# Performance work log

Hardware: AMD Instinct MI355X
Metric: run time of the kernel (lower is better)

Reference implementation:

```python
import jax, jax.numpy as jnp
import numpy as np


def setup_inputs() -> dict:
    key = jax.random.key(0)
    ks = jax.random.split(key, 7)
    B, P, D = 32, 576, 768   # batch, tokens (24x24 patches), inp_dim
    H, HD = 12, 64           # n_heads, head_dim = inp_dim // n_heads
    s = 0.02
    return {
        "x": jax.random.normal(ks[0], (B, P, D), dtype=jnp.float32),
        "Wq": jax.random.normal(ks[1], (H, D, HD), dtype=jnp.float32) * s,
        "bq": jax.random.normal(ks[2], (H, HD), dtype=jnp.float32) * s,
        "Wk": jax.random.normal(ks[3], (H, D, HD), dtype=jnp.float32) * s,
        "bk": jax.random.normal(ks[4], (H, HD), dtype=jnp.float32) * s,
        "Wv": jax.random.normal(ks[5], (H, D, HD), dtype=jnp.float32) * s,
        "bv": jax.random.normal(ks[6], (H, HD), dtype=jnp.float32) * s,
    }


def reference(x, Wq, bq, Wk, bk, Wv, bv):
    # Per-head independent linear projections (stacked over head axis h).
    # x: [b, p, d]; Wq/Wk/Wv: [h, d, k]; biases: [h, k]
    q = jnp.einsum("bpd,hdk->bhpk", x, Wq) + bq[None, :, None, :]
    k = jnp.einsum("bpd,hdk->bhpk", x, Wk) + bk[None, :, None, :]
    v = jnp.einsum("bpd,hdk->bhpk", x, Wv) + bv[None, :, None, :]
    head_dim = k.shape[-1]
    scale = 1.0 / jnp.sqrt(jnp.asarray(head_dim, dtype=x.dtype))
    attn = jnp.einsum("bhqk,bhpk->bhqp", q, k) * scale  # [b, h, p, p]
    attn = jax.nn.softmax(attn, axis=-1)
    out = jnp.einsum("bhqp,bhpk->bhqk", attn, v)        # [b, h, p, k]
    b, h, p, hd = out.shape
    # concat heads along last dim (dropout is identity in eval mode)
    return jnp.transpose(out, (0, 2, 1, 3)).reshape(b, p, h * hd)
```

## Files before the change

### kernel.cpp

```cpp
#include <hip/hip_runtime.h>

typedef unsigned short ushort_t;
typedef unsigned int u32;
typedef float f32x4 __attribute__((ext_vector_type(4)));
typedef short short8 __attribute__((ext_vector_type(8)));

#define NB 32
#define NP 576
#define ND 768
#define NH 12
#define NHD 64

#define WT_BYTES  (36*64*768*2)
#define KV_BYTES  (32*12*576*64*2)
#define QSCALE    0.18033688f

static __device__ __forceinline__ ushort_t f2bf(float f) {
    return __builtin_bit_cast(ushort_t, (__bf16)f);
}
static __device__ __forceinline__ short8 pack8(float4 a, float4 b) {
    union { ushort_t u[8]; short8 v; } pk;
    pk.u[0]=f2bf(a.x); pk.u[1]=f2bf(a.y); pk.u[2]=f2bf(a.z); pk.u[3]=f2bf(a.w);
    pk.u[4]=f2bf(b.x); pk.u[5]=f2bf(b.y); pk.u[6]=f2bf(b.z); pk.u[7]=f2bf(b.w);
    return pk.v;
}
static __device__ __forceinline__ void gl_lds16(const ushort_t* g, ushort_t* l) {
    __builtin_amdgcn_global_load_lds((const __attribute__((address_space(1))) u32*)g,
                                     (__attribute__((address_space(3))) u32*)l, 16, 0, 0);
}
static __device__ __forceinline__ int swzb(int row, int chunk) {
    return row * 128 + (((chunk ^ (row & 7)) & 7) << 4);
}
#define MFMA16 __builtin_amdgcn_mfma_f32_16x16x32_bf16

__global__ __launch_bounds__(256) void prep_w(
    const float* __restrict__ Wq, const float* __restrict__ Wk,
    const float* __restrict__ Wv, ushort_t* __restrict__ Wt)
{
    int idx = blockIdx.x * 256 + threadIdx.x;
    int d0   = (idx % 96) * 8;
    int rest = idx / 96;
    int hd   = rest & 63;
    int ph   = rest >> 6;
    int h    = ph % 12, pr = ph / 12;
    const float* W = (pr == 0) ? Wq : (pr == 1 ? Wk : Wv);
    union { ushort_t u[8]; short8 v; } pk;
    #pragma unroll
    for (int j = 0; j < 8; ++j)
        pk.u[j] = f2bf(W[(size_t)(h * 768 + d0 + j) * 64 + hd]);
    *(short8*)(Wt + ((size_t)(ph * 64 + hd)) * 768 + d0) = pk.v;
}

__global__ __launch_bounds__(256) void proj_qkv(
    const float* __restrict__ x, const ushort_t* __restrict__ Wt,
    const float* __restrict__ bq, const float* __restrict__ bk,
    const float* __restrict__ bv,
    ushort_t* __restrict__ Qb, ushort_t* __restrict__ Kb,
    ushort_t* __restrict__ Vtb, int nts, int ph_base)
{
    __shared__ ushort_t smem[22528];

    const int t = threadIdx.x;
    const int w = t >> 6, l = t & 63, m16 = l & 15, g = l >> 4;
    const int wm = w >> 1, wn = w & 1;

    int L = blockIdx.y * gridDim.x + blockIdx.x;
    int xcd = L & 7, jj_ = L >> 3;
    int nt = jj_ % nts, mt = (jj_ / nts) * 8 + xcd;
    const int m0 = mt * 96;
    const int b  = mt / 6, pb = (mt % 6) * 96;

    const int grow = l >> 3, gch = (l & 7) ^ grow;

    float4 ar[3][2];
    auto loadA = [&](int kc) {
        #pragma unroll
        for (int q = 0; q < 3; ++q) {
            int c = t + q * 256, row = c >> 3, ch = c & 7;
            const float4* xp = (const float4*)(x + (size_t)(m0 + row) * 768 + kc * 64 + ch * 8);
            ar[q][0] = xp[0]; ar[q][1] = xp[1];
        }
    };
    auto writeA = [&]() {
        #pragma unroll
        for (int q = 0; q < 3; ++q) {
            int c = t + q * 256, row = c >> 3, ch = c & 7;
            *(short8*)((char*)smem + swzb(row, ch)) = pack8(ar[q][0], ar[q][1]);
        }
    };
    auto stageB = [&](int kc, int d) {
        #pragma unroll
        for (int c4 = 0; c4 < 4; ++c4) {
            int ci = w * 4 + c4;
            const ushort_t* gs = Wt + (size_t)(ph_base * 64 + nt * 128 + ci * 8 + grow) * 768
                               + kc * 64 + gch * 8;
            gl_lds16(gs, smem + 6144 + d * 8192 + ci * 512);
        }
    };

    f32x4 acc[3][4] = {};

    loadA(0); stageB(0, 0); writeA();
    __syncthreads();

    for (int kc = 0; kc < 12; ++kc) {
        const int d = kc & 1;
        if (kc < 11) { loadA(kc + 1); stageB(kc + 1, d ^ 1); }
        __builtin_amdgcn_s_setprio(1);
        #pragma unroll
        for (int jj = 0; jj < 2; ++jj) {
            short8 af[3], bf[4];
            #pragma unroll
            for (int mi = 0; mi < 3; ++mi)
                af[mi] = *(const short8*)((char*)smem + swzb(wm * 48 + mi * 16 + m16, jj * 4 + g));
            #pragma unroll
            for (int ni = 0; ni < 4; ++ni)
                bf[ni] = *(const short8*)((char*)smem + 12288 + d * 16384 + swzb(wn * 64 + ni * 16 + m16, jj * 4 + g));
            #pragma unroll
            for (int mi = 0; mi < 3; ++mi)
                #pragma unroll
                for (int ni = 0; ni < 4; ++ni)
                    acc[mi][ni] = MFMA16(af[mi], bf[ni], acc[mi][ni], 0, 0, 0);
        }
        __builtin_amdgcn_s_setprio(0);
        __syncthreads();
        if (kc < 11) {
            writeA();
            __syncthreads();
        }
    }

    const int ph = ph_base + nt * 2 + wn;
    const int proj = ph / 12, h = ph % 12;
    const float* bias = (proj == 0 ? bq : (proj == 1 ? bk : bv)) + h * 64;
    const float qs = (proj == 0) ? QSCALE : 1.0f;
    ushort_t* sE = smem + w * 4608;

    #pragma unroll
    for (int ni = 0; ni < 4; ++ni) {
        float bvv = bias[ni * 16 + m16];
        #pragma unroll
        for (int mi = 0; mi < 3; ++mi)
            #pragma unroll
            for (int i = 0; i < 4; ++i) {
                float val = (acc[mi][ni][i] + bvv) * qs;
                int tok = mi * 16 + g * 4 + i;
                int hd  = ni * 16 + m16;
                if (proj < 2) sE[tok * 72 + hd] = f2bf(val);
                else          sE[hd * 72 + tok] = f2bf(val);
            }
    }
    if (proj < 2) {
        ushort_t* dst = (proj == 0 ? Qb : Kb)
                      + ((size_t)(b * 12 + h) * 576 + pb + wm * 48) * 64;
        #pragma unroll
        for (int rr = 0; rr < 6; ++rr) {
            int row = rr * 8 + (l >> 3), ch = l & 7;
            *(short8*)(dst + (size_t)row * 64 + ch * 8) = *(const short8*)&sE[row * 72 + ch * 8];
        }
    } else {
        ushort_t* dst = Vtb + (size_t)(b * 12 + h) * 64 * 576 + pb + wm * 48;
        #pragma unroll
        for (int rr = 0; rr < 8; ++rr) {
            int hd = rr * 8 + (l >> 3), tc = l & 7;
            if (tc < 6)
                *(short8*)(dst + (size_t)hd * 576 + tc * 8) = *(const short8*)&sE[hd * 72 + tc * 8];
        }
    }
}

template<int FUSEQ>
__global__ __launch_bounds__(256) void attn_k(
    const float* __restrict__ x, const ushort_t* __restrict__ Wt,
    const float* __restrict__ bq, const ushort_t* __restrict__ Qb,
    const ushort_t* __restrict__ Kb, const ushort_t* __restrict__ Vtb,
    float* __restrict__ out)
{
    __shared__ ushort_t smem[20480];

    const int t = threadIdx.x;
    const int w = t >> 6, l = t & 63, m16 = l & 15, g = l >> 4;

    int L = blockIdx.y * 9 + blockIdx.x;
    int xcd = L & 7, jj_ = L >> 3;
    int qt = jj_ % 9, bh = (jj_ / 9) * 8 + xcd;
    const int b = bh / 12, h = bh % 12;
    const int p0 = qt * 64;

    const int grow = l >> 3, gch = (l & 7) ^ grow;
    const int spbase = 32768 + w * 2048;

    short8 aq0, aq1;

    if constexpr (FUSEQ) {
        f32x4 acc[4] = {};
        const int row = t >> 2, c16 = (t & 3) * 16;
        auto stage = [&](int kc, int d) {
            const float4* xp = (const float4*)(x + (size_t)(b * 576 + p0 + row) * 768 + kc * 64 + c16);
            float4 u0 = xp[0], u1 = xp[1], u2 = xp[2], u3 = xp[3];
            *(short8*)((char*)smem + d * 8192 + swzb(row, c16 >> 3))       = pack8(u0, u1);
            *(short8*)((char*)smem + d * 8192 + swzb(row, (c16 >> 3) + 1)) = pack8(u2, u3);
            #pragma unroll
            for (int c2 = 0; c2 < 2; ++c2) {
                int ci = w * 2 + c2;
                const ushort_t* gs = Wt + (size_t)(h * 64 + ci * 8 + grow) * 768 + kc * 64 + gch * 8;
                gl_lds16(gs, smem + (16384 + d * 8192 + ci * 1024) / 2);
            }
        };
        stage(0, 0); __syncthreads();
        for (int kc = 0; kc < 12; ++kc) {
            int d = kc & 1;
            if (kc < 11) stage(kc + 1, d ^ 1);
            __builtin_amdgcn_s_setprio(1);
            #pragma unroll
            for (int jj = 0; jj < 2; ++jj) {
                short8 a = *(const short8*)((char*)smem + d * 8192 + swzb(w * 16 + m16, jj * 4 + g));
                #pragma unroll
                for (int f = 0; f < 4; ++f) {
                    short8 bb = *(const short8*)((char*)smem + 16384 + d * 8192 + swzb(f * 16 + m16, jj * 4 + g));
                    acc[f] = MFMA16(a, bb, acc[f], 0, 0, 0);
                }
            }
            __builtin_amdgcn_s_setprio(0);
            __syncthreads();
        }
        #pragma unroll
        for (int f = 0; f < 4; ++f) {
            float bqv = bq[h * 64 + f * 16 + m16];
            #pragma unroll
            for (int i = 0; i < 4; ++i) {
                float val = (acc[f][i] + bqv) * QSCALE;
                int r = g * 4 + i, c = f * 16 + m16;
                *(ushort_t*)((char*)smem + spbase + r * 128
                    + (((((c >> 3) ^ (r & 7)) & 7) << 4) | ((c & 7) << 1))) = f2bf(val);
            }
        }
        aq0 = *(const short8*)((char*)smem + spbase + m16 * 128 + (((g ^ (m16 & 7)) & 7) << 4));
        aq1 = *(const short8*)((char*)smem + spbase + m16 * 128 + ((((4 + g) ^ (m16 & 7)) & 7) << 4));
    } else {
        const ushort_t* qsrc = Qb + ((size_t)bh * 576 + p0 + w * 16 + m16) * 64 + g * 8;
        aq0 = *(const short8*)qsrc;
        aq1 = *(const short8*)(qsrc + 32);
    }

    const ushort_t* Kbase = Kb  + (size_t)bh * (576 * 64);
    const ushort_t* Vbase = Vtb + (size_t)bh * (64 * 576);

    auto stageKV = [&](int kt, int d) {
        #pragma unroll
        for (int c2 = 0; c2 < 2; ++c2) {
            int ci = w * 2 + c2;
            gl_lds16(Kbase + (size_t)(kt * 64 + ci * 8 + grow) * 64 + gch * 8,
                     smem + (d * 8192 + ci * 1024) / 2);
            gl_lds16(Vbase + (size_t)(ci * 8 + grow) * 576 + kt * 64 + gch * 8,
                     smem + (16384 + d * 8192 + ci * 1024) / 2);
        }
    };

    float psum[4] = {0.f, 0.f, 0.f, 0.f};
    f32x4 accO[4] = {};

    stageKV(0, 0); __syncthreads();
    for (int kt = 0; kt < 9; ++kt) {
        int d = kt & 1;
        if (kt < 8) stageKV(kt + 1, d ^ 1);

        f32x4 s[4] = {};
        __builtin_amdgcn_s_setprio(1);
        #pragma unroll
        for (int jj = 0; jj < 2; ++jj) {
            short8 aqj = jj ? aq1 : aq0;
            #pragma unroll
            for (int f = 0; f < 4; ++f) {
                short8 bk_ = *(const short8*)((char*)smem + d * 8192 + swzb(f * 16 + m16, jj * 4 + g));
                s[f] = MFMA16(aqj, bk_, s[f], 0, 0, 0);
            }
        }
        __builtin_amdgcn_s_setprio(0);

        #pragma unroll
        for (int f = 0; f < 4; ++f)
            #pragma unroll
            for (int i = 0; i < 4; ++i) {
                float p = exp2f(s[f][i]);
                s[f][i] = p;
                psum[i] += p;
            }

        #pragma unroll
        for (int f = 0; f < 4; ++f)
            #pragma unroll
            for (int i = 0; i < 4; ++i) {
                int r = g * 4 + i, c = f * 16 + m16;
                *(ushort_t*)((char*)smem + spbase + r * 128
                    + (((((c >> 3) ^ (r & 7)) & 7) << 4) | ((c & 7) << 1))) = f2bf(s[f][i]);
            }
        short8 pa0 = *(const short8*)((char*)smem + spbase + m16 * 128 + (((g ^ (m16 & 7)) & 7) << 4));
        short8 pa1 = *(const short8*)((char*)smem + spbase + m16 * 128 + ((((4 + g) ^ (m16 & 7)) & 7) << 4));

        __builtin_amdgcn_s_setprio(1);
        #pragma unroll
        for (int jj = 0; jj < 2; ++jj) {
            short8 paj = jj ? pa1 : pa0;
            #pragma unroll
            for (int f = 0; f < 4; ++f) {
                short8 bv_ = *(const short8*)((char*)smem + 16384 + d * 8192 + swzb(f * 16 + m16, jj * 4 + g));
                accO[f] = MFMA16(paj, bv_, accO[f], 0, 0, 0);
            }
        }
        __builtin_amdgcn_s_setprio(0);
        __syncthreads();
    }

    #pragma unroll
    for (int xm = 1; xm < 16; xm <<= 1)
        #pragma unroll
        for (int i = 0; i < 4; ++i)
            psum[i] += __shfl_xor(psum[i], xm, 64);

    float inv[4];
    #pragma unroll
    for (int i = 0; i < 4; ++i) inv[i] = 1.0f / psum[i];
    float* orow = out + ((size_t)b * 576 + p0 + w * 16) * 768 + h * 64;
    #pragma unroll
    for (int f = 0; f < 4; ++f)
        #pragma unroll
        for (int i = 0; i < 4; ++i)
            orow[(size_t)(g * 4 + i) * 768 + f * 16 + m16] = accO[f][i] * inv[i];
}

extern "C" void kernel_launch(void* const* d_in, const int* in_sizes, int n_in,
                              void* d_out, int out_size, void* d_ws, size_t ws_size,
                              hipStream_t stream) {
    const float* x  = (const float*)d_in[0];
    const float* Wq = (const float*)d_in[1];
    const float* bq = (const float*)d_in[2];
    const float* Wk = (const float*)d_in[3];
    const float* bk = (const float*)d_in[4];
    const float* Wv = (const float*)d_in[5];
    const float* bv = (const float*)d_in[6];
    float* out = (float*)d_out;

    ushort_t* Wt  = (ushort_t*)d_ws;
    ushort_t* Kb  = (ushort_t*)((char*)d_ws + WT_BYTES);
    ushort_t* Vtb = (ushort_t*)((char*)d_ws + WT_BYTES + KV_BYTES);
    ushort_t* Qb  = (ushort_t*)((char*)d_ws + WT_BYTES + 2 * (size_t)KV_BYTES);

    const bool bigws = ws_size >= (size_t)WT_BYTES + 3 * (size_t)KV_BYTES;

    hipLaunchKernelGGL(prep_w, dim3(864), dim3(256), 0, stream, Wq, Wk, Wv, Wt);
    if (bigws) {
        hipLaunchKernelGGL(proj_qkv, dim3(18, 192), dim3(256), 0, stream,
                           x, Wt, bq, bk, bv, Qb, Kb, Vtb, 18, 0);
        hipLaunchKernelGGL((attn_k<0>), dim3(9, 384), dim3(256), 0, stream,
                           x, Wt, bq, Qb, Kb, Vtb, out);
    } else {
        hipLaunchKernelGGL(proj_qkv, dim3(12, 192), dim3(256), 0, stream,
                           x, Wt, bq, bk, bv, Qb, Kb, Vtb, 12, 12);
        hipLaunchKernelGGL((attn_k<1>), dim3(9, 384), dim3(256), 0, stream,
                           x, Wt, bq, Qb, Kb, Vtb, out);
    }
}
```

Before: 196.5 us.

## Pre-convert x to bf16, fuse Q projection into attention, use async-staged KV projection

Adds a prep pass that converts x to bf16 alongside the weight transpose. The K/V projection becomes a 128x128-tile kernel that loads both operands with global_load_lds. The Q projection is dropped from the projection kernel and computed inside the attention kernel from the bf16 x via async loads. This removes the Q round-trip through memory and the fp32 x reloads with in-register conversion, at the cost of an extra bf16 copy of x and a non-double-buffered projection loop.

```diff
diff --git a/kernel.cpp b/kernel.cpp
--- a/kernel.cpp
+++ b/kernel.cpp
@@ -5,13 +5,8 @@
 typedef float f32x4 __attribute__((ext_vector_type(4)));
 typedef short short8 __attribute__((ext_vector_type(8)));
 
-#define NB 32
-#define NP 576
-#define ND 768
-#define NH 12
-#define NHD 64
-
 #define WT_BYTES  (36*64*768*2)
+#define XB_BYTES  (32*576*768*2)
 #define KV_BYTES  (32*12*576*64*2)
 #define QSCALE    0.18033688f
 
@@ -33,40 +28,145 @@
 }
 #define MFMA16 __builtin_amdgcn_mfma_f32_16x16x32_bf16
 
-__global__ __launch_bounds__(256) void prep_w(
+__global__ __launch_bounds__(256) void prep(
     const float* __restrict__ Wq, const float* __restrict__ Wk,
-    const float* __restrict__ Wv, ushort_t* __restrict__ Wt)
+    const float* __restrict__ Wv, const float* __restrict__ x,
+    ushort_t* __restrict__ Wt, ushort_t* __restrict__ xb)
 {
     int idx = blockIdx.x * 256 + threadIdx.x;
-    int d0   = (idx % 96) * 8;
-    int rest = idx / 96;
-    int hd   = rest & 63;
-    int ph   = rest >> 6;
-    int h    = ph % 12, pr = ph / 12;
-    const float* W = (pr == 0) ? Wq : (pr == 1 ? Wk : Wv);
-    union { ushort_t u[8]; short8 v; } pk;
-    #pragma unroll
-    for (int j = 0; j < 8; ++j)
-        pk.u[j] = f2bf(W[(size_t)(h * 768 + d0 + j) * 64 + hd]);
-    *(short8*)(Wt + ((size_t)(ph * 64 + hd)) * 768 + d0) = pk.v;
-}
-
-__global__ __launch_bounds__(256) void proj_qkv(
-    const float* __restrict__ x, const ushort_t* __restrict__ Wt,
-    const float* __restrict__ bq, const float* __restrict__ bk,
-    const float* __restrict__ bv,
-    ushort_t* __restrict__ Qb, ushort_t* __restrict__ Kb,
-    ushort_t* __restrict__ Vtb, int nts, int ph_base)
+    if (idx < 221184) {
+        int d0   = (idx % 96) * 8;
+        int rest = idx / 96;
+        int hd   = rest & 63;
+        int ph   = rest >> 6;
+        int h    = ph % 12, pr = ph / 12;
+        const float* W = (pr == 0) ? Wq : (pr == 1 ? Wk : Wv);
+        union { ushort_t u[8]; short8 v; } pk;
+        #pragma unroll
+        for (int j = 0; j < 8; ++j)
+            pk.u[j] = f2bf(W[(size_t)(h * 768 + d0 + j) * 64 + hd]);
+        *(short8*)(Wt + ((size_t)(ph * 64 + hd)) * 768 + d0) = pk.v;
+    } else {
+        size_t e = (size_t)(idx - 221184) * 8;
+        const float4* xp = (const float4*)(x + e);
+        *(short8*)(xb + e) = pack8(xp[0], xp[1]);
+    }
+}
+
+__global__ __launch_bounds__(256) void proj_kv(
+    const ushort_t* __restrict__ xb, const ushort_t* __restrict__ Wt,
+    const float* __restrict__ bk, const float* __restrict__ bv,
+    ushort_t* __restrict__ Kb, ushort_t* __restrict__ Vtb)
 {
-    __shared__ ushort_t smem[22528];
+    __shared__ ushort_t smem[18432];
 
     const int t = threadIdx.x;
     const int w = t >> 6, l = t & 63, m16 = l & 15, g = l >> 4;
     const int wm = w >> 1, wn = w & 1;
 
-    int L = blockIdx.y * gridDim.x + blockIdx.x;
+    int L = blockIdx.y * 12 + blockIdx.x;
     int xcd = L & 7, jj_ = L >> 3;
-    int nt = jj_ % nts, mt = (jj_ / nts) * 8 + xcd;
+    int nt = jj_ % 12, mt = (jj_ / 12) * 8 + xcd;
+    const int m0 = mt * 128;
+    const int ph0 = 12 + nt * 2;
+
+    const int grow = l >> 3, gch = (l & 7) ^ grow;
+
+    auto stageA = [&](int kc) {
+        #pragma unroll
+        for (int c4 = 0; c4 < 4; ++c4) {
+            int ci = w * 4 + c4;
+            gl_lds16(xb + (size_t)(m0 + ci * 8 + grow) * 768 + kc * 64 + gch * 8,
+                     smem + ci * 512);
+        }
+    };
+    auto stageB = [&](int kc) {
+        #pragma unroll
+        for (int c4 = 0; c4 < 4; ++c4) {
+            int ci = w * 4 + c4;
+            int r  = ci * 8 + grow;
+            gl_lds16(Wt + ((size_t)(ph0 + (r >> 6)) * 64 + (r & 63)) * 768 + kc * 64 + gch * 8,
+                     smem + 8192 + ci * 512);
+        }
+    };
+
+    f32x4 acc[4][4] = {};
+
+    for (int kc = 0; kc < 12; ++kc) {
+        __syncthreads();
+        stageA(kc); stageB(kc);
+        __syncthreads();
+        __builtin_amdgcn_s_setprio(1);
+        #pragma unroll
+        for (int jj = 0; jj < 2; ++jj) {
+            short8 af[4], bf[4];
+            #pragma unroll
+            for (int mi = 0; mi < 4; ++mi)
+                af[mi] = *(const short8*)((char*)smem + swzb(wm * 64 + mi * 16 + m16, jj * 4 + g));
+            #pragma unroll
+            for (int ni = 0; ni < 4; ++ni)
+                bf[ni] = *(const short8*)((char*)smem + 16384 + swzb(wn * 64 + ni * 16 + m16, jj * 4 + g));
+            #pragma unroll
+            for (int mi = 0; mi < 4; ++mi)
+                #pragma unroll
+                for (int ni = 0; ni < 4; ++ni)
+                    acc[mi][ni] = MFMA16(af[mi], bf[ni], acc[mi][ni], 0, 0, 0);
+        }
+        __builtin_amdgcn_s_setprio(0);
+    }
+    __syncthreads();
+
+    const int ph = ph0 + wn, proj = ph / 12, h = ph % 12;
+    const float* bias = (proj == 1 ? bk : bv) + h * 64;
+    const int tokg0 = m0 + wm * 64;
+    const int bb = tokg0 / 576, pp = tokg0 % 576;
+    ushort_t* sE = smem + w * 4608;
+
+    #pragma unroll
+    for (int ni = 0; ni < 4; ++ni) {
+        float bvv = bias[ni * 16 + m16];
+        #pragma unroll
+        for (int mi = 0; mi < 4; ++mi)
+            #pragma unroll
+            for (int i = 0; i < 4; ++i) {
+                float val = acc[mi][ni][i] + bvv;
+                int tok = mi * 16 + g * 4 + i;
+                int hd  = ni * 16 + m16;
+                if (proj == 1) sE[tok * 72 + hd] = f2bf(val);
+                else           sE[hd * 72 + tok] = f2bf(val);
+            }
+    }
+    if (proj == 1) {
+        ushort_t* dst = Kb + ((size_t)(bb * 12 + h) * 576 + pp) * 64;
+        #pragma unroll
+        for (int rr = 0; rr < 8; ++rr) {
+            int row = rr * 8 + (l >> 3), ch = l & 7;
+            *(short8*)(dst + (size_t)row * 64 + ch * 8) = *(const short8*)&sE[row * 72 + ch * 8];
+        }
+    } else {
+        ushort_t* dst = Vtb + (size_t)(bb * 12 + h) * 64 * 576 + pp;
+        #pragma unroll
+        for (int rr = 0; rr < 8; ++rr) {
+            int hd = rr * 8 + (l >> 3), tc = l & 7;
+            *(short8*)(dst + (size_t)hd * 576 + tc * 8) = *(const short8*)&sE[hd * 72 + tc * 8];
+        }
+    }
+}
+
+__global__ __launch_bounds__(256) void proj_reg(
+    const float* __restrict__ x, const ushort_t* __restrict__ Wt,
+    const float* __restrict__ bk, const float* __restrict__ bv,
+    ushort_t* __restrict__ Kb, ushort_t* __restrict__ Vtb)
+{
+    __shared__ ushort_t smem[22528];
+
+    const int t = threadIdx.x;
+    const int w = t >> 6, l = t & 63, m16 = l & 15, g = l >> 4;
+    const int wm = w >> 1, wn = w & 1;
+
+    int L = blockIdx.y * 12 + blockIdx.x;
+    int xcd = L & 7, jj_ = L >> 3;
+    int nt = jj_ % 12, mt = (jj_ / 12) * 8 + xcd;
     const int m0 = mt * 96;
     const int b  = mt / 6, pb = (mt % 6) * 96;
 
@@ -92,14 +192,13 @@
         #pragma unroll
         for (int c4 = 0; c4 < 4; ++c4) {
             int ci = w * 4 + c4;
-            const ushort_t* gs = Wt + (size_t)(ph_base * 64 + nt * 128 + ci * 8 + grow) * 768
+            const ushort_t* gs = Wt + (size_t)((12 + nt * 2) * 64 + ci * 8 + grow) * 768
                                + kc * 64 + gch * 8;
             gl_lds16(gs, smem + 6144 + d * 8192 + ci * 512);
         }
     };
 
     f32x4 acc[3][4] = {};
-
     loadA(0); stageB(0, 0); writeA();
     __syncthreads();
 
@@ -124,16 +223,12 @@
         }
         __builtin_amdgcn_s_setprio(0);
         __syncthreads();
-        if (kc < 11) {
-            writeA();
-            __syncthreads();
-        }
-    }
-
-    const int ph = ph_base + nt * 2 + wn;
+        if (kc < 11) { writeA(); __syncthreads(); }
+    }
+
+    const int ph = 12 + nt * 2 + wn;
     const int proj = ph / 12, h = ph % 12;
-    const float* bias = (proj == 0 ? bq : (proj == 1 ? bk : bv)) + h * 64;
-    const float qs = (proj == 0) ? QSCALE : 1.0f;
+    const float* bias = (proj == 1 ? bk : bv) + h * 64;
     ushort_t* sE = smem + w * 4608;
 
     #pragma unroll
@@ -143,16 +238,15 @@
         for (int mi = 0; mi < 3; ++mi)
             #pragma unroll
             for (int i = 0; i < 4; ++i) {
-                float val = (acc[mi][ni][i] + bvv) * qs;
+                float val = acc[mi][ni][i] + bvv;
                 int tok = mi * 16 + g * 4 + i;
                 int hd  = ni * 16 + m16;
-                if (proj < 2) sE[tok * 72 + hd] = f2bf(val);
-                else          sE[hd * 72 + tok] = f2bf(val);
-            }
-    }
-    if (proj < 2) {
-        ushort_t* dst = (proj == 0 ? Qb : Kb)
-                      + ((size_t)(b * 12 + h) * 576 + pb + wm * 48) * 64;
+                if (proj == 1) sE[tok * 72 + hd] = f2bf(val);
+                else           sE[hd * 72 + tok] = f2bf(val);
+            }
+    }
+    if (proj == 1) {
+        ushort_t* dst = Kb + ((size_t)(b * 12 + h) * 576 + pb + wm * 48) * 64;
         #pragma unroll
         for (int rr = 0; rr < 6; ++rr) {
             int row = rr * 8 + (l >> 3), ch = l & 7;
@@ -169,10 +263,10 @@
     }
 }
 
-template<int FUSEQ>
+template<int MODE>
 __global__ __launch_bounds__(256) void attn_k(
-    const float* __restrict__ x, const ushort_t* __restrict__ Wt,
-    const float* __restrict__ bq, const ushort_t* __restrict__ Qb,
+    const float* __restrict__ x, const ushort_t* __restrict__ xb,
+    const ushort_t* __restrict__ Wt, const float* __restrict__ bq,
     const ushort_t* __restrict__ Kb, const ushort_t* __restrict__ Vtb,
     float* __restrict__ out)
 {
@@ -191,20 +285,30 @@
     const int spbase = 32768 + w * 2048;
 
     short8 aq0, aq1;
-
-    if constexpr (FUSEQ) {
+    {
         f32x4 acc[4] = {};
-        const int row = t >> 2, c16 = (t & 3) * 16;
         auto stage = [&](int kc, int d) {
-            const float4* xp = (const float4*)(x + (size_t)(b * 576 + p0 + row) * 768 + kc * 64 + c16);
-            float4 u0 = xp[0], u1 = xp[1], u2 = xp[2], u3 = xp[3];
-            *(short8*)((char*)smem + d * 8192 + swzb(row, c16 >> 3))       = pack8(u0, u1);
-            *(short8*)((char*)smem + d * 8192 + swzb(row, (c16 >> 3) + 1)) = pack8(u2, u3);
-            #pragma unroll
-            for (int c2 = 0; c2 < 2; ++c2) {
-                int ci = w * 2 + c2;
-                const ushort_t* gs = Wt + (size_t)(h * 64 + ci * 8 + grow) * 768 + kc * 64 + gch * 8;
-                gl_lds16(gs, smem + (16384 + d * 8192 + ci * 1024) / 2);
+            if constexpr (MODE == 2) {
+                #pragma unroll
+                for (int c2 = 0; c2 < 2; ++c2) {
+                    int ci = w * 2 + c2;
+                    gl_lds16(xb + (size_t)(b * 576 + p0 + ci * 8 + grow) * 768 + kc * 64 + gch * 8,
+                             smem + (d * 8192 + ci * 1024) / 2);
+                    gl_lds16(Wt + (size_t)(h * 64 + ci * 8 + grow) * 768 + kc * 64 + gch * 8,
+                             smem + (16384 + d * 8192 + ci * 1024) / 2);
+                }
+            } else {
+                const int row = t >> 2, c16 = (t & 3) * 16;
+                const float4* xp = (const float4*)(x + (size_t)(b * 576 + p0 + row) * 768 + kc * 64 + c16);
+                float4 u0 = xp[0], u1 = xp[1], u2 = xp[2], u3 = xp[3];
+                *(short8*)((char*)smem + d * 8192 + swzb(row, c16 >> 3))       = pack8(u0, u1);
+                *(short8*)((char*)smem + d * 8192 + swzb(row, (c16 >> 3) + 1)) = pack8(u2, u3);
+                #pragma unroll
+                for (int c2 = 0; c2 < 2; ++c2) {
+                    int ci = w * 2 + c2;
+                    gl_lds16(Wt + (size_t)(h * 64 + ci * 8 + grow) * 768 + kc * 64 + gch * 8,
+                             smem + (16384 + d * 8192 + ci * 1024) / 2);
+                }
             }
         };
         stage(0, 0); __syncthreads();
@@ -237,10 +341,6 @@
         }
         aq0 = *(const short8*)((char*)smem + spbase + m16 * 128 + (((g ^ (m16 & 7)) & 7) << 4));
         aq1 = *(const short8*)((char*)smem + spbase + m16 * 128 + ((((4 + g) ^ (m16 & 7)) & 7) << 4));
-    } else {
-        const ushort_t* qsrc = Qb + ((size_t)bh * 576 + p0 + w * 16 + m16) * 64 + g * 8;
-        aq0 = *(const short8*)qsrc;
-        aq1 = *(const short8*)(qsrc + 32);
     }
 
     const ushort_t* Kbase = Kb  + (size_t)bh * (576 * 64);
@@ -341,23 +441,26 @@
     const float* bv = (const float*)d_in[6];
     float* out = (float*)d_out;
 
-    ushort_t* Wt  = (ushort_t*)d_ws;
-    ushort_t* Kb  = (ushort_t*)((char*)d_ws + WT_BYTES);
-    ushort_t* Vtb = (ushort_t*)((char*)d_ws + WT_BYTES + KV_BYTES);
-    ushort_t* Qb  = (ushort_t*)((char*)d_ws + WT_BYTES + 2 * (size_t)KV_BYTES);
-
-    const bool bigws = ws_size >= (size_t)WT_BYTES + 3 * (size_t)KV_BYTES;
-
-    hipLaunchKernelGGL(prep_w, dim3(864), dim3(256), 0, stream, Wq, Wk, Wv, Wt);
+    const bool bigws = ws_size >= (size_t)WT_BYTES + XB_BYTES + 2 * (size_t)KV_BYTES;
+
     if (bigws) {
-        hipLaunchKernelGGL(proj_qkv, dim3(18, 192), dim3(256), 0, stream,
-                           x, Wt, bq, bk, bv, Qb, Kb, Vtb, 18, 0);
-        hipLaunchKernelGGL((attn_k<0>), dim3(9, 384), dim3(256), 0, stream,
-                           x, Wt, bq, Qb, Kb, Vtb, out);
+        ushort_t* Wt  = (ushort_t*)d_ws;
+        ushort_t* xbp = (ushort_t*)((char*)d_ws + WT_BYTES);
+        ushort_t* Kb  = (ushort_t*)((char*)d_ws + WT_BYTES + XB_BYTES);
+        ushort_t* Vtb = (ushort_t*)((char*)d_ws + WT_BYTES + XB_BYTES + (size_t)KV_BYTES);
+        hipLaunchKernelGGL(prep, dim3(7776), dim3(256), 0, stream, Wq, Wk, Wv, x, Wt, xbp);
+        hipLaunchKernelGGL(proj_kv, dim3(12, 144), dim3(256), 0, stream,
+                           xbp, Wt, bk, bv, Kb, Vtb);
+        hipLaunchKernelGGL((attn_k<2>), dim3(9, 384), dim3(256), 0, stream,
+                           x, xbp, Wt, bq, Kb, Vtb, out);
     } else {
-        hipLaunchKernelGGL(proj_qkv, dim3(12, 192), dim3(256), 0, stream,
-                           x, Wt, bq, bk, bv, Qb, Kb, Vtb, 12, 12);
+        ushort_t* Wt  = (ushort_t*)d_ws;
+        ushort_t* Kb  = (ushort_t*)((char*)d_ws + WT_BYTES);
+        ushort_t* Vtb = (ushort_t*)((char*)d_ws + WT_BYTES + (size_t)KV_BYTES);
+        hipLaunchKernelGGL(prep, dim3(864), dim3(256), 0, stream, Wq, Wk, Wv, x, Wt, (ushort_t*)nullptr);
+        hipLaunchKernelGGL(proj_reg, dim3(12, 192), dim3(256), 0, stream,
+                           x, Wt, bk, bv, Kb, Vtb);
         hipLaunchKernelGGL((attn_k<1>), dim3(9, 384), dim3(256), 0, stream,
-                           x, Wt, bq, Qb, Kb, Vtb, out);
-    }
-}
+                           x, (const ushort_t*)nullptr, Wt, bq, Kb, Vtb, out);
+    }
+}
```

After: 180.9 us. -7.9%, faster.
